# Kernel optimization log

Hardware: AMD Instinct MI355X
Metric: run time of the kernel (lower is better)

## Reference

```python
import jax, jax.numpy as jnp
import numpy as np

WCNT, EMB, H, T, B = 50000, 25, 25, 200, 4096


def setup_inputs() -> dict:
    key = jax.random.key(0)
    ks = jax.random.split(key, 12)
    s = 1.0 / np.sqrt(H)  # PyTorch GRU init range

    def u(k, shape):
        return jax.random.uniform(k, shape, minval=-s, maxval=s, dtype=jnp.float32)

    emb = jax.random.normal(ks[1], (WCNT, EMB), dtype=jnp.float32)
    emb = emb.at[0].set(0.0)  # padding_idx=0
    return {
        "input": jax.random.randint(ks[0], (T, B), 0, WCNT),
        "hidden": jnp.zeros((2, B, H), jnp.float32),
        "emb": emb,
        "w_ih_f": u(ks[2], (3 * H, EMB)), "w_hh_f": u(ks[3], (3 * H, H)),
        "b_ih_f": u(ks[4], (3 * H,)),     "b_hh_f": u(ks[5], (3 * H,)),
        "w_ih_b": u(ks[6], (3 * H, EMB)), "w_hh_b": u(ks[7], (3 * H, H)),
        "b_ih_b": u(ks[8], (3 * H,)),     "b_hh_b": u(ks[9], (3 * H,)),
    }


def _gru_dir(x, h0, w_ih, w_hh, b_ih, b_hh, reverse):
    # Precompute input-gate projections for all timesteps: [T, B, 3H]
    xg = jnp.einsum('tbi,gi->tbg', x, w_ih) + b_ih

    def step(h, xg_t):
        gh = h @ w_hh.T + b_hh
        xr, xz, xn = jnp.split(xg_t, 3, axis=-1)
        hr, hz, hn = jnp.split(gh, 3, axis=-1)
        r = jax.nn.sigmoid(xr + hr)
        z = jax.nn.sigmoid(xz + hz)
        n = jnp.tanh(xn + r * hn)
        h_new = (1.0 - z) * n + z * h
        return h_new, h_new

    hT, ys = jax.lax.scan(step, h0, xg, reverse=reverse)
    return ys, hT  # ys in original time order even when reversed


def reference(input, hidden, emb,
              w_ih_f, w_hh_f, b_ih_f, b_hh_f,
              w_ih_b, w_hh_b, b_ih_b, b_hh_b):
    emb_eff = emb.at[0].set(0.0)          # padding_idx=0
    x = emb_eff[input]                    # [T, B, EMB]
    yf, hf = _gru_dir(x, hidden[0], w_ih_f, w_hh_f, b_ih_f, b_hh_f, False)
    yb, hb = _gru_dir(x, hidden[1], w_ih_b, w_hh_b, b_ih_b, b_hh_b, True)
    y = jnp.concatenate([yf, yb], axis=-1)  # [T, B, 2H]
    y = jnp.max(y, axis=0)                  # max over time -> [B, 2H]
    h = jnp.stack([hf, hb], axis=0)         # [2, B, H]
    return (y, h)
```

## Files before the change

kernel.cpp:

```cpp
#include <hip/hip_runtime.h>
#include <cstddef>

#define T_LEN 200
#define BATCH 4096
#define EMBD  25
#define HD    25
#define WCNT  50000

__device__ __forceinline__ float frcp(float x) {
#if __has_builtin(__builtin_amdgcn_rcpf)
    return __builtin_amdgcn_rcpf(x);
#else
    return 1.0f / x;
#endif
}

__device__ __forceinline__ float fsig(float x) {
    float e = __expf(-x);
    return frcp(1.0f + e);
}
__device__ __forceinline__ float ftanh_(float x) {
    float e = __expf(-2.0f * x);
    return (1.0f - e) * frcp(1.0f + e);
}

__global__ __launch_bounds__(256) void embp_kernel(
    const float* __restrict__ emb,
    const float* __restrict__ w_ih_f, const float* __restrict__ b_ih_f,
    const float* __restrict__ w_ih_b, const float* __restrict__ b_ih_b,
    float* __restrict__ embP)
{
    int tid = blockIdx.x * 256 + threadIdx.x;
    if (tid >= 2 * WCNT * HD) return;
    int i   = tid % HD;
    int w   = (tid / HD) % WCNT;
    int dir = tid / (HD * WCNT);
    const float* wih = dir ? w_ih_b : w_ih_f;
    const float* bih = dir ? b_ih_b : b_ih_f;
    const float* er  = emb + (size_t)w * EMBD;
    const float* w0  = wih + (0 * HD + i) * EMBD;
    const float* w1  = wih + (1 * HD + i) * EMBD;
    const float* w2  = wih + (2 * HD + i) * EMBD;
    float a0 = bih[i], a1 = bih[HD + i], a2 = bih[2 * HD + i];
    #pragma unroll
    for (int j = 0; j < EMBD; ++j) {
        float x = er[j];
        a0 = fmaf(w0[j], x, a0);
        a1 = fmaf(w1[j], x, a1);
        a2 = fmaf(w2[j], x, a2);
    }
    float* o = embP + ((size_t)dir * WCNT + w) * 75 + i * 3;
    o[0] = a0; o[1] = a1; o[2] = a2;
}

__global__ __launch_bounds__(256, 4) void gru_embp_kernel(
    const int*   __restrict__ input,
    const float* __restrict__ hidden,
    const float* __restrict__ w_hh_f, const float* __restrict__ b_hh_f,
    const float* __restrict__ w_hh_b, const float* __restrict__ b_hh_b,
    const float* __restrict__ embP,
    float* __restrict__ out)
{
    __shared__ float hsh[8][28];

    const int wave = threadIdx.x >> 6;
    const int half = (threadIdx.x >> 5) & 1;
    const int sub  = threadIdx.x & 31;
    const int b    = blockIdx.x * 4 + wave;
    const int dir  = half;
    const int csub = sub < 25 ? sub : 0;
    const int c    = wave * 2 + half;

    const float* whh = dir ? w_hh_b : w_hh_f;
    const float* bhh = dir ? b_hh_b : b_hh_f;

    float wg0[25], wg1[25], wg2[25];
    #pragma unroll
    for (int j = 0; j < 25; ++j) {
        wg0[j] = whh[(0 * 25 + csub) * 25 + j];
        wg1[j] = whh[(1 * 25 + csub) * 25 + j];
        wg2[j] = whh[(2 * 25 + csub) * 25 + j];
    }
    const float bh0 = bhh[csub], bh1 = bhh[25 + csub], bh2 = bhh[50 + csub];

    float h0 = 0.0f;
    if (sub < 25) h0 = hidden[((size_t)dir * BATCH + b) * HD + sub];
    if (sub < 25) hsh[c][sub] = h0;
    __syncthreads();

    const int* ipt  = input + (dir ? (T_LEN - 1) * BATCH : 0) + b;
    const int  istr = dir ? -BATCH : BATCH;

    int ia = ipt[0];
    int ib_ = ipt[istr];
    int ic = ipt[2 * istr];
    int id_ = ipt[3 * istr];

    const float* tbl = embP + (size_t)dir * WCNT * 75 + csub * 3;

    float xa0, xa1, xa2, xb0, xb1, xb2;
    {
        const float* p = tbl + (size_t)ia * 75;
        xa0 = p[0]; xa1 = p[1]; xa2 = p[2];
        const float* q = tbl + (size_t)ib_ * 75;
        xb0 = q[0]; xb1 = q[1]; xb2 = q[2];
    }

    float hown = h0;
    float ymax = -3.0e38f;
    const float4* h4 = (const float4*)(&hsh[c][0]);

    #pragma unroll 2
    for (int tt = 0; tt < T_LEN; ++tt) {
        float xc0, xc1, xc2;
        {
            const float* p = tbl + (size_t)ic * 75;
            xc0 = p[0]; xc1 = p[1]; xc2 = p[2];
        }
        ic = id_;
        int t4 = (tt + 4 < T_LEN) ? tt + 4 : T_LEN - 1;
        id_ = ipt[t4 * istr];

        float ar = bh0, az = bh1, an = bh2;
        #pragma unroll
        for (int jb = 0; jb < 6; ++jb) {
            float4 hv = h4[jb];
            ar = fmaf(wg0[4*jb+0], hv.x, ar); ar = fmaf(wg0[4*jb+1], hv.y, ar);
            ar = fmaf(wg0[4*jb+2], hv.z, ar); ar = fmaf(wg0[4*jb+3], hv.w, ar);
            az = fmaf(wg1[4*jb+0], hv.x, az); az = fmaf(wg1[4*jb+1], hv.y, az);
            az = fmaf(wg1[4*jb+2], hv.z, az); az = fmaf(wg1[4*jb+3], hv.w, az);
            an = fmaf(wg2[4*jb+0], hv.x, an); an = fmaf(wg2[4*jb+1], hv.y, an);
            an = fmaf(wg2[4*jb+2], hv.z, an); an = fmaf(wg2[4*jb+3], hv.w, an);
        }
        float h24 = hsh[c][24];
        ar = fmaf(wg0[24], h24, ar);
        az = fmaf(wg1[24], h24, az);
        an = fmaf(wg2[24], h24, an);

        float r = fsig(xa0 + ar);
        float z = fsig(xa1 + az);
        float n = ftanh_(fmaf(r, an, xa2));
        float hnew = fmaf(z, hown - n, n);
        ymax = fmaxf(ymax, hnew);

        __builtin_amdgcn_wave_barrier();
        if (sub < 25) hsh[c][sub] = hnew;
        __builtin_amdgcn_wave_barrier();

        hown = hnew;
        xa0 = xb0; xa1 = xb1; xa2 = xb2;
        xb0 = xc0; xb1 = xc1; xb2 = xc2;
    }

    if (sub < 25) {
        out[(size_t)b * 50 + dir * 25 + sub] = ymax;
        out[204800 + ((size_t)dir * BATCH + b) * HD + sub] = hown;
    }
}

__global__ __launch_bounds__(256) void gru_fallback_kernel(
    const int*   __restrict__ input,
    const float* __restrict__ hidden,
    const float* __restrict__ emb,
    const float* __restrict__ w_hh_f, const float* __restrict__ b_hh_f,
    const float* __restrict__ w_ih_f, const float* __restrict__ b_ih_f,
    const float* __restrict__ w_hh_b, const float* __restrict__ b_hh_b,
    const float* __restrict__ w_ih_b, const float* __restrict__ b_ih_b,
    float* __restrict__ out)
{
    __shared__ float4 hsh4[8][7];
    __shared__ float4 xsh4[8][7];
    float* hshf = (float*)hsh4;
    float* xshf = (float*)xsh4;

    const int wave = threadIdx.x >> 6;
    const int half = (threadIdx.x >> 5) & 1;
    const int sub  = threadIdx.x & 31;
    const int b    = blockIdx.x * 4 + wave;
    const int dir  = half;
    const int csub = sub < 25 ? sub : 0;
    const int c    = wave * 2 + half;

    const float* whh = dir ? w_hh_b : w_hh_f;
    const float* bhh = dir ? b_hh_b : b_hh_f;
    const float* wih = dir ? w_ih_b : w_ih_f;
    const float* bih = dir ? b_ih_b : b_ih_f;

    float wg0[28], wg1[28], wg2[28], wi0[28], wi1[28], wi2[28];
    #pragma unroll
    for (int j = 0; j < 28; ++j) {
        wg0[j] = (j < 25) ? whh[(0 * 25 + csub) * 25 + j] : 0.0f;
        wg1[j] = (j < 25) ? whh[(1 * 25 + csub) * 25 + j] : 0.0f;
        wg2[j] = (j < 25) ? whh[(2 * 25 + csub) * 25 + j] : 0.0f;
        wi0[j] = (j < 25) ? wih[(0 * 25 + csub) * 25 + j] : 0.0f;
        wi1[j] = (j < 25) ? wih[(1 * 25 + csub) * 25 + j] : 0.0f;
        wi2[j] = (j < 25) ? wih[(2 * 25 + csub) * 25 + j] : 0.0f;
    }
    const float bh0 = bhh[csub], bh1 = bhh[25 + csub], bh2 = bhh[50 + csub];
    const float bx0 = bih[csub], bx1 = bih[25 + csub], bx2 = bih[50 + csub];

    float h0 = 0.0f;
    if (sub < 25) h0 = hidden[((size_t)dir * BATCH + b) * HD + sub];
    if (sub < 28) hshf[c * 28 + sub] = (sub < 25) ? h0 : 0.0f;
    if (sub >= 25 && sub < 28) xshf[c * 28 + sub] = 0.0f;
    __syncthreads();

    const int* ipt  = input + (dir ? (T_LEN - 1) * BATCH : 0) + b;
    const int  istr = dir ? -BATCH : BATCH;

    int idx_c = ipt[0];
    int idx_n = ipt[istr];
    float xcur = emb[(size_t)idx_c * EMBD + csub];

    float hown = h0;
    float ymax = -3.0e38f;

    for (int tt = 0; tt < T_LEN; ++tt) {
        int t2 = (tt + 2 < T_LEN) ? tt + 2 : T_LEN - 1;
        int idx_n2 = ipt[t2 * istr];
        float xnext = emb[(size_t)idx_n * EMBD + csub];
        __builtin_amdgcn_wave_barrier();
        if (sub < 25) xshf[c * 28 + sub] = xcur;
        __builtin_amdgcn_wave_barrier();

        float ar = bh0, az = bh1, an = bh2;
        float axr = bx0, axz = bx1, axn = bx2;
        #pragma unroll
        for (int jb = 0; jb < 7; ++jb) {
            float4 hv = hsh4[c][jb];
            float4 xv = xsh4[c][jb];
            ar = fmaf(wg0[4*jb+0], hv.x, ar); ar = fmaf(wg0[4*jb+1], hv.y, ar);
            ar = fmaf(wg0[4*jb+2], hv.z, ar); ar = fmaf(wg0[4*jb+3], hv.w, ar);
            az = fmaf(wg1[4*jb+0], hv.x, az); az = fmaf(wg1[4*jb+1], hv.y, az);
            az = fmaf(wg1[4*jb+2], hv.z, az); az = fmaf(wg1[4*jb+3], hv.w, az);
            an = fmaf(wg2[4*jb+0], hv.x, an); an = fmaf(wg2[4*jb+1], hv.y, an);
            an = fmaf(wg2[4*jb+2], hv.z, an); an = fmaf(wg2[4*jb+3], hv.w, an);
            axr = fmaf(wi0[4*jb+0], xv.x, axr); axr = fmaf(wi0[4*jb+1], xv.y, axr);
            axr = fmaf(wi0[4*jb+2], xv.z, axr); axr = fmaf(wi0[4*jb+3], xv.w, axr);
            axz = fmaf(wi1[4*jb+0], xv.x, axz); axz = fmaf(wi1[4*jb+1], xv.y, axz);
            axz = fmaf(wi1[4*jb+2], xv.z, axz); axz = fmaf(wi1[4*jb+3], xv.w, axz);
            axn = fmaf(wi2[4*jb+0], xv.x, axn); axn = fmaf(wi2[4*jb+1], xv.y, axn);
            axn = fmaf(wi2[4*jb+2], xv.z, axn); axn = fmaf(wi2[4*jb+3], xv.w, axn);
        }

        float r = fsig(axr + ar);
        float z = fsig(axz + az);
        float n = ftanh_(fmaf(r, an, axn));
        float hnew = fmaf(z, hown - n, n);
        ymax = fmaxf(ymax, hnew);

        __builtin_amdgcn_wave_barrier();
        if (sub < 25) hshf[c * 28 + sub] = hnew;
        __builtin_amdgcn_wave_barrier();

        hown = hnew;
        xcur = xnext;
        idx_c = idx_n; idx_n = idx_n2;
    }

    if (sub < 25) {
        out[(size_t)b * 50 + dir * 25 + sub] = ymax;
        out[204800 + ((size_t)dir * BATCH + b) * HD + sub] = hown;
    }
}

extern "C" void kernel_launch(void* const* d_in, const int* in_sizes, int n_in,
                              void* d_out, int out_size, void* d_ws, size_t ws_size,
                              hipStream_t stream) {
    const int*   input  = (const int*)  d_in[0];
    const float* hidden = (const float*)d_in[1];
    const float* emb    = (const float*)d_in[2];
    const float* w_ih_f = (const float*)d_in[3];
    const float* w_hh_f = (const float*)d_in[4];
    const float* b_ih_f = (const float*)d_in[5];
    const float* b_hh_f = (const float*)d_in[6];
    const float* w_ih_b = (const float*)d_in[7];
    const float* w_hh_b = (const float*)d_in[8];
    const float* b_ih_b = (const float*)d_in[9];
    const float* b_hh_b = (const float*)d_in[10];
    float* out = (float*)d_out;

    const size_t embp_bytes = (size_t)2 * WCNT * 75 * sizeof(float);
    if (ws_size >= embp_bytes) {
        float* embP = (float*)d_ws;
        int total = 2 * WCNT * HD;
        embp_kernel<<<(total + 255) / 256, 256, 0, stream>>>(
            emb, w_ih_f, b_ih_f, w_ih_b, b_ih_b, embP);
        gru_embp_kernel<<<BATCH / 4, 256, 0, stream>>>(
            input, hidden,
            w_hh_f, b_hh_f, w_hh_b, b_hh_b,
            embP, out);
    } else {
        gru_fallback_kernel<<<BATCH / 4, 256, 0, stream>>>(
            input, hidden, emb,
            w_hh_f, b_hh_f, w_ih_f, b_ih_f,
            w_hh_b, b_hh_b, w_ih_b, b_ih_b,
            out);
    }
}
```

Measured before the change: 268.0 us.

## Split hidden-state dot product across half-waves and re-layout projected embedding table

```diff
diff --git a/kernel.cpp b/kernel.cpp
--- a/kernel.cpp
+++ b/kernel.cpp
@@ -24,36 +24,51 @@
     return (1.0f - e) * frcp(1.0f + e);
 }
 
-__global__ __launch_bounds__(256) void embp_kernel(
+__device__ __forceinline__ float bperm_f(int bpidx, float v) {
+    return __int_as_float(__builtin_amdgcn_ds_bpermute(bpidx, __float_as_int(v)));
+}
+
+__global__ __launch_bounds__(256) void embp2_kernel(
     const float* __restrict__ emb,
     const float* __restrict__ w_ih_f, const float* __restrict__ b_ih_f,
     const float* __restrict__ w_ih_b, const float* __restrict__ b_ih_b,
     float* __restrict__ embP)
 {
-    int tid = blockIdx.x * 256 + threadIdx.x;
-    if (tid >= 2 * WCNT * HD) return;
-    int i   = tid % HD;
-    int w   = (tid / HD) % WCNT;
-    int dir = tid / (HD * WCNT);
+    __shared__ float esh[256 * EMBD];
+    const int dir = blockIdx.y;
+    const int w0  = blockIdx.x * 256;
+    const int tid = threadIdx.x;
+
+    for (int k = tid; k < 256 * EMBD; k += 256) {
+        int g = w0 * EMBD + k;
+        esh[k] = (g < WCNT * EMBD) ? emb[g] : 0.0f;
+    }
+    __syncthreads();
+
+    const int w = w0 + tid;
+    if (w >= WCNT) return;
     const float* wih = dir ? w_ih_b : w_ih_f;
     const float* bih = dir ? b_ih_b : b_ih_f;
-    const float* er  = emb + (size_t)w * EMBD;
-    const float* w0  = wih + (0 * HD + i) * EMBD;
-    const float* w1  = wih + (1 * HD + i) * EMBD;
-    const float* w2  = wih + (2 * HD + i) * EMBD;
-    float a0 = bih[i], a1 = bih[HD + i], a2 = bih[2 * HD + i];
+
+    float er[EMBD];
     #pragma unroll
-    for (int j = 0; j < EMBD; ++j) {
-        float x = er[j];
-        a0 = fmaf(w0[j], x, a0);
-        a1 = fmaf(w1[j], x, a1);
-        a2 = fmaf(w2[j], x, a2);
-    }
-    float* o = embP + ((size_t)dir * WCNT + w) * 75 + i * 3;
-    o[0] = a0; o[1] = a1; o[2] = a2;
-}
-
-__global__ __launch_bounds__(256, 4) void gru_embp_kernel(
+    for (int j = 0; j < EMBD; ++j) er[j] = esh[tid * EMBD + j];
+
+    for (int i = 0; i < HD; ++i) {
+        float a0 = bih[i], a1 = bih[HD + i], a2 = bih[2 * HD + i];
+        #pragma unroll
+        for (int j = 0; j < EMBD; ++j) {
+            float x = er[j];
+            a0 = fmaf(wih[(0 * HD + i) * EMBD + j], x, a0);
+            a1 = fmaf(wih[(1 * HD + i) * EMBD + j], x, a1);
+            a2 = fmaf(wih[(2 * HD + i) * EMBD + j], x, a2);
+        }
+        float* o = embP + (((size_t)dir * HD + i) * WCNT + w) * 3;
+        o[0] = a0; o[1] = a1; o[2] = a2;
+    }
+}
+
+__global__ __launch_bounds__(256) void gru3_kernel(
     const int*   __restrict__ input,
     const float* __restrict__ hidden,
     const float* __restrict__ w_hh_f, const float* __restrict__ b_hh_f,
@@ -61,100 +76,112 @@
     const float* __restrict__ embP,
     float* __restrict__ out)
 {
-    __shared__ float hsh[8][28];
-
-    const int wave = threadIdx.x >> 6;
-    const int half = (threadIdx.x >> 5) & 1;
-    const int sub  = threadIdx.x & 31;
-    const int b    = blockIdx.x * 4 + wave;
-    const int dir  = half;
-    const int csub = sub < 25 ? sub : 0;
-    const int c    = wave * 2 + half;
+    __shared__ float hsh[4][28];
+
+    const int tid  = threadIdx.x;
+    const int wid  = __builtin_amdgcn_readfirstlane(tid >> 6);
+    const int lane = tid & 63;
+    const int jh   = lane >> 5;
+    const int l    = lane & 31;
+    const int csub = l < 25 ? l : 0;
+    const int chain = blockIdx.x * 4 + wid;
+    const int b    = chain >> 1;
+    const int dir  = chain & 1;
 
     const float* whh = dir ? w_hh_b : w_hh_f;
     const float* bhh = dir ? b_hh_b : b_hh_f;
 
-    float wg0[25], wg1[25], wg2[25];
+    const int jo = jh * 12;
+    float wq0[13], wq1[13], wq2[13];
     #pragma unroll
-    for (int j = 0; j < 25; ++j) {
-        wg0[j] = whh[(0 * 25 + csub) * 25 + j];
-        wg1[j] = whh[(1 * 25 + csub) * 25 + j];
-        wg2[j] = whh[(2 * 25 + csub) * 25 + j];
-    }
-    const float bh0 = bhh[csub], bh1 = bhh[25 + csub], bh2 = bhh[50 + csub];
-
-    float h0 = 0.0f;
-    if (sub < 25) h0 = hidden[((size_t)dir * BATCH + b) * HD + sub];
-    if (sub < 25) hsh[c][sub] = h0;
-    __syncthreads();
-
-    const int* ipt  = input + (dir ? (T_LEN - 1) * BATCH : 0) + b;
-    const int  istr = dir ? -BATCH : BATCH;
-
-    int ia = ipt[0];
-    int ib_ = ipt[istr];
-    int ic = ipt[2 * istr];
-    int id_ = ipt[3 * istr];
-
-    const float* tbl = embP + (size_t)dir * WCNT * 75 + csub * 3;
-
-    float xa0, xa1, xa2, xb0, xb1, xb2;
+    for (int k = 0; k < 13; ++k) {
+        wq0[k] = whh[(0 * 25 + csub) * 25 + jo + k];
+        wq1[k] = whh[(1 * 25 + csub) * 25 + jo + k];
+        wq2[k] = whh[(2 * 25 + csub) * 25 + jo + k];
+    }
+    if (jh) { wq0[0] = 0.f; wq1[0] = 0.f; wq2[0] = 0.f; }
+    const float bh0 = jh ? 0.f : bhh[csub];
+    const float bh1 = jh ? 0.f : bhh[25 + csub];
+    const float bh2 = jh ? 0.f : bhh[50 + csub];
+
+    float h0v = 0.f;
+    if (l < 25) h0v = hidden[((size_t)dir * BATCH + b) * HD + l];
+    if (jh == 0 && l < 25) hsh[wid][l] = h0v;
+    __builtin_amdgcn_wave_barrier();
+
+    const char* hb = (const char*)&hsh[wid][0] + jh * 48;
+
+    int t0 = dir ? (T_LEN - 1) : 0;
+    int t1 = dir ? (T_LEN - 2) : 1;
+    int si_c = input[t0 * BATCH + b];
+    int si_n = input[t1 * BATCH + b];
+
+    const float* dbase = embP + (size_t)dir * HD * WCNT * 3;
+    const unsigned lane_off = (unsigned)csub * WCNT * 3;
+
+    float3 xg;
     {
-        const float* p = tbl + (size_t)ia * 75;
-        xa0 = p[0]; xa1 = p[1]; xa2 = p[2];
-        const float* q = tbl + (size_t)ib_ * 75;
-        xb0 = q[0]; xb1 = q[1]; xb2 = q[2];
-    }
-
-    float hown = h0;
+        const float* p = dbase + lane_off + (unsigned)si_c * 3;
+        xg.x = p[0]; xg.y = p[1]; xg.z = p[2];
+    }
+
+    const int bpidx = (lane ^ 32) << 2;
+    float hown = h0v;
     float ymax = -3.0e38f;
-    const float4* h4 = (const float4*)(&hsh[c][0]);
 
     #pragma unroll 2
     for (int tt = 0; tt < T_LEN; ++tt) {
-        float xc0, xc1, xc2;
+        float3 xgn;
         {
-            const float* p = tbl + (size_t)ic * 75;
-            xc0 = p[0]; xc1 = p[1]; xc2 = p[2];
+            const float* p = dbase + lane_off + (unsigned)si_n * 3;
+            xgn.x = p[0]; xgn.y = p[1]; xgn.z = p[2];
         }
-        ic = id_;
-        int t4 = (tt + 4 < T_LEN) ? tt + 4 : T_LEN - 1;
-        id_ = ipt[t4 * istr];
+        int tpre = (tt + 2 < T_LEN) ? tt + 2 : T_LEN - 1;
+        int trow = dir ? (T_LEN - 1 - tpre) : tpre;
+        int si_n2 = input[trow * BATCH + b];
+
+        float4 hv0 = *(const float4*)(hb);
+        float4 hv1 = *(const float4*)(hb + 16);
+        float4 hv2 = *(const float4*)(hb + 32);
+        float h12  = *(const float*)(hb + 48);
 
         float ar = bh0, az = bh1, an = bh2;
-        #pragma unroll
-        for (int jb = 0; jb < 6; ++jb) {
-            float4 hv = h4[jb];
-            ar = fmaf(wg0[4*jb+0], hv.x, ar); ar = fmaf(wg0[4*jb+1], hv.y, ar);
-            ar = fmaf(wg0[4*jb+2], hv.z, ar); ar = fmaf(wg0[4*jb+3], hv.w, ar);
-            az = fmaf(wg1[4*jb+0], hv.x, az); az = fmaf(wg1[4*jb+1], hv.y, az);
-            az = fmaf(wg1[4*jb+2], hv.z, az); az = fmaf(wg1[4*jb+3], hv.w, az);
-            an = fmaf(wg2[4*jb+0], hv.x, an); an = fmaf(wg2[4*jb+1], hv.y, an);
-            an = fmaf(wg2[4*jb+2], hv.z, an); an = fmaf(wg2[4*jb+3], hv.w, an);
-        }
-        float h24 = hsh[c][24];
-        ar = fmaf(wg0[24], h24, ar);
-        az = fmaf(wg1[24], h24, az);
-        an = fmaf(wg2[24], h24, an);
-
-        float r = fsig(xa0 + ar);
-        float z = fsig(xa1 + az);
-        float n = ftanh_(fmaf(r, an, xa2));
+        ar = fmaf(wq0[0], hv0.x, ar); az = fmaf(wq1[0], hv0.x, az); an = fmaf(wq2[0], hv0.x, an);
+        ar = fmaf(wq0[1], hv0.y, ar); az = fmaf(wq1[1], hv0.y, az); an = fmaf(wq2[1], hv0.y, an);
+        ar = fmaf(wq0[2], hv0.z, ar); az = fmaf(wq1[2], hv0.z, az); an = fmaf(wq2[2], hv0.z, an);
+        ar = fmaf(wq0[3], hv0.w, ar); az = fmaf(wq1[3], hv0.w, az); an = fmaf(wq2[3], hv0.w, an);
+        ar = fmaf(wq0[4], hv1.x, ar); az = fmaf(wq1[4], hv1.x, az); an = fmaf(wq2[4], hv1.x, an);
+        ar = fmaf(wq0[5], hv1.y, ar); az = fmaf(wq1[5], hv1.y, az); an = fmaf(wq2[5], hv1.y, an);
+        ar = fmaf(wq0[6], hv1.z, ar); az = fmaf(wq1[6], hv1.z, az); an = fmaf(wq2[6], hv1.z, an);
+        ar = fmaf(wq0[7], hv1.w, ar); az = fmaf(wq1[7], hv1.w, az); an = fmaf(wq2[7], hv1.w, an);
+        ar = fmaf(wq0[8], hv2.x, ar); az = fmaf(wq1[8], hv2.x, az); an = fmaf(wq2[8], hv2.x, an);
+        ar = fmaf(wq0[9], hv2.y, ar); az = fmaf(wq1[9], hv2.y, az); an = fmaf(wq2[9], hv2.y, an);
+        ar = fmaf(wq0[10], hv2.z, ar); az = fmaf(wq1[10], hv2.z, az); an = fmaf(wq2[10], hv2.z, an);
+        ar = fmaf(wq0[11], hv2.w, ar); az = fmaf(wq1[11], hv2.w, az); an = fmaf(wq2[11], hv2.w, an);
+        ar = fmaf(wq0[12], h12, ar);  az = fmaf(wq1[12], h12, az);  an = fmaf(wq2[12], h12, an);
+
+        ar += bperm_f(bpidx, ar);
+        az += bperm_f(bpidx, az);
+        an += bperm_f(bpidx, an);
+
+        float r = fsig(xg.x + ar);
+        float z = fsig(xg.y + az);
+        float n = ftanh_(fmaf(r, an, xg.z));
         float hnew = fmaf(z, hown - n, n);
         ymax = fmaxf(ymax, hnew);
 
         __builtin_amdgcn_wave_barrier();
-        if (sub < 25) hsh[c][sub] = hnew;
+        if (jh == 0 && l < 25) hsh[wid][l] = hnew;
         __builtin_amdgcn_wave_barrier();
 
         hown = hnew;
-        xa0 = xb0; xa1 = xb1; xa2 = xb2;
-        xb0 = xc0; xb1 = xc1; xb2 = xc2;
-    }
-
-    if (sub < 25) {
-        out[(size_t)b * 50 + dir * 25 + sub] = ymax;
-        out[204800 + ((size_t)dir * BATCH + b) * HD + sub] = hown;
+        xg = xgn;
+        si_n = si_n2;
+    }
+
+    if (jh == 0 && l < 25) {
+        out[(size_t)b * 50 + dir * 25 + l] = ymax;
+        out[204800 + ((size_t)dir * BATCH + b) * HD + l] = hown;
     }
 }
 
@@ -280,13 +307,13 @@
     const float* b_hh_b = (const float*)d_in[10];
     float* out = (float*)d_out;
 
-    const size_t embp_bytes = (size_t)2 * WCNT * 75 * sizeof(float);
+    const size_t embp_bytes = (size_t)2 * HD * WCNT * 3 * sizeof(float);
     if (ws_size >= embp_bytes) {
         float* embP = (float*)d_ws;
-        int total = 2 * WCNT * HD;
-        embp_kernel<<<(total + 255) / 256, 256, 0, stream>>>(
+        dim3 grid((WCNT + 255) / 256, 2);
+        embp2_kernel<<<grid, 256, 0, stream>>>(
             emb, w_ih_f, b_ih_f, w_ih_b, b_ih_b, embP);
-        gru_embp_kernel<<<BATCH / 4, 256, 0, stream>>>(
+        gru3_kernel<<<(2 * BATCH) / 4, 256, 0, stream>>>(
             input, hidden,
             w_hh_f, b_hh_f, w_hh_b, b_hh_b,
             embP, out);
```

After: 792.2 us. 196% more time.
